# Kernel optimization log

Measured on AMD Instinct MI355X. Metric: run time of the kernel, lower is better.

Reference implementation:

```python
import jax, jax.numpy as jnp
import numpy as np

N, D, H = 8192, 64, 128
GRID = 256
RADIUS2 = 9  # radius=3 squared


def setup_inputs() -> dict:
    key = jax.random.key(0)
    ks = jax.random.split(key, 9)
    s = lambda k, shape, scale: jax.random.normal(k, shape, dtype=jnp.float32) * scale
    return {
        "positions": jax.random.randint(ks[0], (N, 2), 0, GRID, dtype=jnp.int32),
        "states": s(ks[1], (N, D), 0.1),
        "h": s(ks[2], (N, H), 0.1),
        "c": s(ks[3], (N, H), 0.1),
        "W_ih": s(ks[4], (4 * H, 2 * D), 1.0 / np.sqrt(2 * D)),
        "W_hh": s(ks[5], (4 * H, H), 1.0 / np.sqrt(H)),
        "b": s(ks[6], (4 * H,), 0.01),
        "W_out": s(ks[7], (H, D), 1.0 / np.sqrt(H)),
        "W_role": s(ks[8], (H, 3), 1.0 / np.sqrt(H)),
    }


def reference(positions, states, h, c, W_ih, W_hh, b, W_out, W_role):
    # --- neighbor gather: all-pairs distance on integer grid, radius 3 ---
    d = positions[:, None, :] - positions[None, :, :]          # [N,N,2]
    dist2 = jnp.sum(d * d, axis=-1)                            # [N,N] int32
    mask = (dist2 <= RADIUS2) & (~jnp.eye(N, dtype=bool))      # exclude self
    maskf = mask.astype(states.dtype)
    cnt = jnp.sum(maskf, axis=1, keepdims=True)                # [N,1]
    # mean of neighbor states; zeros when no neighbors (matches zeros fallback)
    nbr_mean = (maskf @ states) / jnp.maximum(cnt, 1.0)        # [N,D]

    # --- per-cell LSTM memory update ---
    x = jnp.concatenate([states, nbr_mean], axis=-1)           # [N,2D]
    gates = x @ W_ih.T + h @ W_hh.T + b                        # [N,4H]
    i_g, f_g, g_g, o_g = jnp.split(gates, 4, axis=-1)
    c_new = jax.nn.sigmoid(f_g) * c + jax.nn.sigmoid(i_g) * jnp.tanh(g_g)
    h_new = jax.nn.sigmoid(o_g) * jnp.tanh(c_new)              # [N,H]

    new_states = h_new @ W_out                                 # [N,D]
    role_probs = jax.nn.softmax(h_new @ W_role, axis=-1)       # [N,3]
    return new_states, role_probs
```

## Files before the change

kernel.cpp:

```cpp
#include <hip/hip_runtime.h>
#include <hip/hip_bf16.h>
#include <math.h>

#define N_CELLS 8192
#define D_DIM 64
#define H_DIM 128
#define GRID_SZ 256
#define NBINS (GRID_SZ * GRID_SZ)
#define BUCKET_CAP 16

typedef short bf16x8 __attribute__((ext_vector_type(8)));
typedef float f32x4 __attribute__((ext_vector_type(4)));

static __device__ __forceinline__ short f2bf(float x) {
    __hip_bfloat16 b = __float2bfloat16(x);
    return __builtin_bit_cast(short, b);
}

__global__ __launch_bounds__(256) void clear_counts(int4* __restrict__ counts4) {
    counts4[blockIdx.x * 256 + threadIdx.x] = make_int4(0, 0, 0, 0);
}

__global__ __launch_bounds__(256) void bin_fill(const int* __restrict__ positions,
                                                int* __restrict__ counts,
                                                int* __restrict__ buckets) {
    int i = blockIdx.x * 256 + threadIdx.x;
    if (i >= N_CELLS) return;
    int p0 = positions[2 * i], p1 = positions[2 * i + 1];
    int bin = p0 * GRID_SZ + p1;
    int slot = atomicAdd(&counts[bin], 1);
    if (slot < BUCKET_CAP) buckets[bin * BUCKET_CAP + slot] = i;
}

__global__ __launch_bounds__(256) void build_xh_wcvt(const int* __restrict__ positions,
                                                     const float* __restrict__ states,
                                                     const float* __restrict__ h,
                                                     const int* __restrict__ counts,
                                                     const int* __restrict__ buckets,
                                                     const float* __restrict__ Wih,
                                                     const float* __restrict__ Whh,
                                                     __hip_bfloat16* __restrict__ xh,
                                                     __hip_bfloat16* __restrict__ Wb) {
    int tid = threadIdx.x;
    if (blockIdx.x >= 2048) {
        int idx4 = (blockIdx.x - 2048) * 256 + tid;
        int gp = idx4 >> 6, k4 = (idx4 & 63) << 2;
        int group = gp >> 6, c6 = gp & 63, gate = c6 >> 4, hl = c6 & 15;
        int orig = gate * 128 + group * 16 + hl;
        float4 v = (k4 < 128) ? *(const float4*)(Wih + orig * 128 + k4)
                              : *(const float4*)(Whh + orig * 128 + (k4 - 128));
        short4 o = make_short4(f2bf(v.x), f2bf(v.y), f2bf(v.z), f2bf(v.w));
        *(short4*)((short*)Wb + gp * 256 + k4) = o;
        return;
    }
    int wave = tid >> 6;
    int lane = tid & 63;
    int i = blockIdx.x * 4 + wave;
    int p0 = positions[2 * i], p1 = positions[2 * i + 1];

    float acc = 0.0f;
    int cnt = 0;
    #pragma unroll
    for (int da = -3; da <= 3; ++da) {
        int q0 = p0 + da;
        if (q0 < 0 || q0 >= GRID_SZ) continue;
        int maxdb2 = 9 - da * da;
        #pragma unroll
        for (int db = -3; db <= 3; ++db) {
            if (db * db > maxdb2) continue;
            int q1 = p1 + db;
            if (q1 < 0 || q1 >= GRID_SZ) continue;
            int bin = q0 * GRID_SZ + q1;
            int c = counts[bin];
            if (c > BUCKET_CAP) c = BUCKET_CAP;
            for (int s = 0; s < c; ++s) {
                int j = buckets[bin * BUCKET_CAP + s];
                if (j == i) continue;
                cnt++;
                acc += states[j * D_DIM + lane];
            }
        }
    }
    float nbr = (cnt > 0) ? acc / (float)cnt : 0.0f;

    __hip_bfloat16* row = xh + (size_t)i * 256;
    row[lane]       = __float2bfloat16(states[i * D_DIM + lane]);
    row[64 + lane]  = __float2bfloat16(nbr);
    row[128 + lane] = __float2bfloat16(h[i * H_DIM + lane]);
    row[192 + lane] = __float2bfloat16(h[i * H_DIM + 64 + lane]);
}

__global__ __launch_bounds__(512) void mega(const __hip_bfloat16* __restrict__ xh,
                                            const __hip_bfloat16* __restrict__ Wb,
                                            const float* __restrict__ bias,
                                            const float* __restrict__ c_in,
                                            const float* __restrict__ W_out,
                                            const float* __restrict__ W_role,
                                            float* __restrict__ out) {
    __shared__ char smem[69632];
    char* As = smem;
    char* Bs = smem + 4096;
    char* Hl   = smem;
    char* Wohi = smem + 8192;
    char* Wolo = smem + 24576;
    char* Wr   = smem + 40960;

    const int tid  = threadIdx.x;
    const int lane = tid & 63;
    const int wid  = tid >> 6;
    const int wrow = wid >> 2, wcol = wid & 3;
    const int n0 = blockIdx.x * 32;

    const char* aG = (const char*)xh;
    const char* bG = (const char*)Wb;

    f32x4 acc[8] = {};

    for (int kc = 0; kc < 4; ++kc) {
        if (kc) __syncthreads();
        if (tid < 256) {
            int row = tid >> 3, slot = (tid & 7) << 4;
            __builtin_amdgcn_global_load_lds(
                (const __attribute__((address_space(1))) void*)(aG + (size_t)(n0 + row) * 512 + kc * 128 + (slot ^ ((row & 7) << 4))),
                (__attribute__((address_space(3))) void*)(As + row * 128 + slot), 16, 0, 0);
        }
        #pragma unroll
        for (int e = 0; e < 8; ++e) {
            int u = e * 512 + tid;
            int row = u >> 3, slot = (u & 7) << 4;
            __builtin_amdgcn_global_load_lds(
                (const __attribute__((address_space(1))) void*)(bG + (size_t)row * 512 + kc * 128 + (slot ^ ((row & 7) << 4))),
                (__attribute__((address_space(3))) void*)(Bs + row * 128 + slot), 16, 0, 0);
        }
        __syncthreads();

        #pragma unroll
        for (int ks = 0; ks < 2; ++ks) {
            int kb = ks * 64 + ((lane >> 4) << 4);
            int arow = wrow * 16 + (lane & 15);
            bf16x8 av = *(const bf16x8*)(As + arow * 128 + (kb ^ ((arow & 7) << 4)));
            #pragma unroll
            for (int ni = 0; ni < 8; ++ni) {
                int brow = wcol * 128 + ni * 16 + (lane & 15);
                bf16x8 bv = *(const bf16x8*)(Bs + brow * 128 + (kb ^ ((brow & 7) << 4)));
                acc[ni] = __builtin_amdgcn_mfma_f32_16x16x32_bf16(av, bv, acc[ni], 0, 0, 0);
            }
        }
    }
    __syncthreads();

    #pragma unroll
    for (int e = 0; e < 16; ++e) {
        int u = e * 512 + tid;
        int hh = u >> 6, d = u & 63;
        float w = W_out[u];
        float whi = __bfloat162float(__float2bfloat16(w));
        int off = d * 256 + ((hh * 2) ^ ((d & 7) << 4));
        *(short*)(Wohi + off) = f2bf(whi);
        *(short*)(Wolo + off) = f2bf(w - whi);
    }
    #pragma unroll
    for (int e = 0; e < 4; ++e) {
        int u = e * 512 + tid;
        int r = u >> 7, hh = u & 127;
        float w = (r < 3) ? W_role[hh * 3 + r] : 0.0f;
        *(short*)(Wr + r * 256 + ((hh * 2) ^ ((r & 7) << 4))) = f2bf(w);
    }

    #pragma unroll
    for (int b = 0; b < 2; ++b) {
        int hg = (2 * wcol + b) * 16 + (lane & 15);
        float bi = bias[hg], bff = bias[128 + hg], bgg = bias[256 + hg], boo = bias[384 + hg];
        #pragma unroll
        for (int r = 0; r < 4; ++r) {
            int ml = wrow * 16 + ((lane >> 4) << 2) + r;
            float ig = acc[b * 4 + 0][r] + bi;
            float fg = acc[b * 4 + 1][r] + bff;
            float gg = acc[b * 4 + 2][r] + bgg;
            float og = acc[b * 4 + 3][r] + boo;
            float cv = c_in[(size_t)(n0 + ml) * H_DIM + hg];
            float si = 1.0f / (1.0f + expf(-ig));
            float sf = 1.0f / (1.0f + expf(-fg));
            float so = 1.0f / (1.0f + expf(-og));
            float hn = so * tanhf(sf * cv + si * tanhf(gg));
            *(short*)(Hl + ml * 256 + ((hg * 2) ^ ((ml & 7) << 4))) = f2bf(hn);
        }
    }
    __syncthreads();

    const int rb = wid >> 2, db = wid & 3;
    f32x4 oacc = {};
    f32x4 racc = {};
    #pragma unroll
    for (int ks = 0; ks < 4; ++ks) {
        int kb = ks * 64 + ((lane >> 4) << 4);
        int hrow = rb * 16 + (lane & 15);
        bf16x8 hv = *(const bf16x8*)(Hl + hrow * 256 + (kb ^ ((hrow & 7) << 4)));
        int drow = db * 16 + (lane & 15);
        int woff = drow * 256 + (kb ^ ((drow & 7) << 4));
        bf16x8 whi = *(const bf16x8*)(Wohi + woff);
        bf16x8 wlo = *(const bf16x8*)(Wolo + woff);
        oacc = __builtin_amdgcn_mfma_f32_16x16x32_bf16(hv, whi, oacc, 0, 0, 0);
        oacc = __builtin_amdgcn_mfma_f32_16x16x32_bf16(hv, wlo, oacc, 0, 0, 0);
        if (db == 3) {
            int rrow = lane & 15;
            bf16x8 wr = *(const bf16x8*)(Wr + rrow * 256 + (kb ^ ((rrow & 7) << 4)));
            racc = __builtin_amdgcn_mfma_f32_16x16x32_bf16(wr, hv, racc, 0, 0, 0);
        }
    }
    #pragma unroll
    for (int r = 0; r < 4; ++r) {
        int m = n0 + rb * 16 + ((lane >> 4) << 2) + r;
        out[(size_t)m * D_DIM + db * 16 + (lane & 15)] = oacc[r];
    }
    if (db == 3 && lane < 16) {
        int m = n0 + rb * 16 + lane;
        float l0 = racc[0], l1 = racc[1], l2 = racc[2];
        float mx = fmaxf(l0, fmaxf(l1, l2));
        float e0 = expf(l0 - mx), e1 = expf(l1 - mx), e2 = expf(l2 - mx);
        float s = e0 + e1 + e2;
        float* ro = out + (size_t)N_CELLS * D_DIM + (size_t)m * 3;
        ro[0] = e0 / s; ro[1] = e1 / s; ro[2] = e2 / s;
    }
}

extern "C" void kernel_launch(void* const* d_in, const int* in_sizes, int n_in,
                              void* d_out, int out_size, void* d_ws, size_t ws_size,
                              hipStream_t stream) {
    const int*   positions = (const int*)d_in[0];
    const float* states    = (const float*)d_in[1];
    const float* h         = (const float*)d_in[2];
    const float* c         = (const float*)d_in[3];
    const float* Wih       = (const float*)d_in[4];
    const float* Whh       = (const float*)d_in[5];
    const float* bias      = (const float*)d_in[6];
    const float* Wout      = (const float*)d_in[7];
    const float* Wrole     = (const float*)d_in[8];
    float* out             = (float*)d_out;

    char* ws = (char*)d_ws;
    int*            counts  = (int*)ws;
    int*            buckets = (int*)(ws + 262144);
    __hip_bfloat16* xh      = (__hip_bfloat16*)(ws + 4456448);
    __hip_bfloat16* Wb      = (__hip_bfloat16*)(ws + 8650752);

    clear_counts<<<NBINS / 1024, 256, 0, stream>>>((int4*)counts);
    bin_fill<<<N_CELLS / 256, 256, 0, stream>>>(positions, counts, buckets);
    build_xh_wcvt<<<2048 + 128, 256, 0, stream>>>(positions, states, h, counts, buckets,
                                                  Wih, Whh, xh, Wb);
    mega<<<N_CELLS / 32, 512, 0, stream>>>(xh, Wb, bias, c, Wout, Wrole, out);
}
```

Measured before the change: 40.92 us.

## Fuse neighbor gather into GEMM kernel and merge weight conversion with count clearing

The neighbor-mean gather and xh row construction move into the mega kernel, which now writes bf16 A-tiles for all 32 rows and the full K=256 directly into LDS instead of staging them through a global xh buffer. Weight conversion is combined with count clearing in a single prep kernel, cutting the launches from four to three and removing the global write and re-read of xh. The cost is larger LDS use per block (80KB), which may limit occupancy, and the gather latency now sits at the start of the GEMM kernel with fewer waves available to hide it.

```diff
diff --git a/kernel.cpp b/kernel.cpp
--- a/kernel.cpp
+++ b/kernel.cpp
@@ -17,8 +17,23 @@
     return __builtin_bit_cast(short, b);
 }
 
-__global__ __launch_bounds__(256) void clear_counts(int4* __restrict__ counts4) {
-    counts4[blockIdx.x * 256 + threadIdx.x] = make_int4(0, 0, 0, 0);
+__global__ __launch_bounds__(256) void prep(const float* __restrict__ Wih,
+                                            const float* __restrict__ Whh,
+                                            __hip_bfloat16* __restrict__ Wb,
+                                            int4* __restrict__ counts4) {
+    int tid = threadIdx.x;
+    if (blockIdx.x >= 128) {
+        counts4[(blockIdx.x - 128) * 256 + tid] = make_int4(0, 0, 0, 0);
+        return;
+    }
+    int idx4 = blockIdx.x * 256 + tid;
+    int gp = idx4 >> 6, k4 = (idx4 & 63) << 2;
+    int group = gp >> 6, c6 = gp & 63, gate = c6 >> 4, hl = c6 & 15;
+    int orig = gate * 128 + group * 16 + hl;
+    float4 v = (k4 < 128) ? *(const float4*)(Wih + orig * 128 + k4)
+                          : *(const float4*)(Whh + orig * 128 + (k4 - 128));
+    short4 o = make_short4(f2bf(v.x), f2bf(v.y), f2bf(v.z), f2bf(v.w));
+    *(short4*)((short*)Wb + gp * 256 + k4) = o;
 }
 
 __global__ __launch_bounds__(256) void bin_fill(const int* __restrict__ positions,
@@ -32,74 +47,20 @@
     if (slot < BUCKET_CAP) buckets[bin * BUCKET_CAP + slot] = i;
 }
 
-__global__ __launch_bounds__(256) void build_xh_wcvt(const int* __restrict__ positions,
-                                                     const float* __restrict__ states,
-                                                     const float* __restrict__ h,
-                                                     const int* __restrict__ counts,
-                                                     const int* __restrict__ buckets,
-                                                     const float* __restrict__ Wih,
-                                                     const float* __restrict__ Whh,
-                                                     __hip_bfloat16* __restrict__ xh,
-                                                     __hip_bfloat16* __restrict__ Wb) {
-    int tid = threadIdx.x;
-    if (blockIdx.x >= 2048) {
-        int idx4 = (blockIdx.x - 2048) * 256 + tid;
-        int gp = idx4 >> 6, k4 = (idx4 & 63) << 2;
-        int group = gp >> 6, c6 = gp & 63, gate = c6 >> 4, hl = c6 & 15;
-        int orig = gate * 128 + group * 16 + hl;
-        float4 v = (k4 < 128) ? *(const float4*)(Wih + orig * 128 + k4)
-                              : *(const float4*)(Whh + orig * 128 + (k4 - 128));
-        short4 o = make_short4(f2bf(v.x), f2bf(v.y), f2bf(v.z), f2bf(v.w));
-        *(short4*)((short*)Wb + gp * 256 + k4) = o;
-        return;
-    }
-    int wave = tid >> 6;
-    int lane = tid & 63;
-    int i = blockIdx.x * 4 + wave;
-    int p0 = positions[2 * i], p1 = positions[2 * i + 1];
-
-    float acc = 0.0f;
-    int cnt = 0;
-    #pragma unroll
-    for (int da = -3; da <= 3; ++da) {
-        int q0 = p0 + da;
-        if (q0 < 0 || q0 >= GRID_SZ) continue;
-        int maxdb2 = 9 - da * da;
-        #pragma unroll
-        for (int db = -3; db <= 3; ++db) {
-            if (db * db > maxdb2) continue;
-            int q1 = p1 + db;
-            if (q1 < 0 || q1 >= GRID_SZ) continue;
-            int bin = q0 * GRID_SZ + q1;
-            int c = counts[bin];
-            if (c > BUCKET_CAP) c = BUCKET_CAP;
-            for (int s = 0; s < c; ++s) {
-                int j = buckets[bin * BUCKET_CAP + s];
-                if (j == i) continue;
-                cnt++;
-                acc += states[j * D_DIM + lane];
-            }
-        }
-    }
-    float nbr = (cnt > 0) ? acc / (float)cnt : 0.0f;
-
-    __hip_bfloat16* row = xh + (size_t)i * 256;
-    row[lane]       = __float2bfloat16(states[i * D_DIM + lane]);
-    row[64 + lane]  = __float2bfloat16(nbr);
-    row[128 + lane] = __float2bfloat16(h[i * H_DIM + lane]);
-    row[192 + lane] = __float2bfloat16(h[i * H_DIM + 64 + lane]);
-}
-
-__global__ __launch_bounds__(512) void mega(const __hip_bfloat16* __restrict__ xh,
+__global__ __launch_bounds__(512) void mega(const int* __restrict__ positions,
+                                            const float* __restrict__ states,
+                                            const float* __restrict__ h,
+                                            const int* __restrict__ counts,
+                                            const int* __restrict__ buckets,
                                             const __hip_bfloat16* __restrict__ Wb,
                                             const float* __restrict__ bias,
                                             const float* __restrict__ c_in,
                                             const float* __restrict__ W_out,
                                             const float* __restrict__ W_role,
                                             float* __restrict__ out) {
-    __shared__ char smem[69632];
+    __shared__ char smem[81920];
     char* As = smem;
-    char* Bs = smem + 4096;
+    char* Bs = smem + 16384;
     char* Hl   = smem;
     char* Wohi = smem + 8192;
     char* Wolo = smem + 24576;
@@ -111,19 +72,54 @@
     const int wrow = wid >> 2, wcol = wid & 3;
     const int n0 = blockIdx.x * 32;
 
-    const char* aG = (const char*)xh;
+    const int DA[29] = {-3,-2,-2,-2,-2,-2,-1,-1,-1,-1,-1, 0, 0, 0, 0, 0, 0, 0, 1, 1, 1, 1, 1, 2, 2, 2, 2, 2, 3};
+    const int DB[29] = { 0,-2,-1, 0, 1, 2,-2,-1, 0, 1, 2,-3,-2,-1, 0, 1, 2, 3,-2,-1, 0, 1, 2,-2,-1, 0, 1, 2, 0};
+
+    #pragma unroll
+    for (int cc = 0; cc < 4; ++cc) {
+        int i = n0 + wid * 4 + cc;
+        int p0 = positions[2 * i], p1 = positions[2 * i + 1];
+        int bc[29], bbase[29];
+        #pragma unroll
+        for (int t = 0; t < 29; ++t) {
+            int q0 = p0 + DA[t], q1 = p1 + DB[t];
+            bool ok = ((unsigned)q0 < GRID_SZ) && ((unsigned)q1 < GRID_SZ);
+            int bin = q0 * GRID_SZ + q1;
+            bc[t] = ok ? counts[bin] : 0;
+            bbase[t] = bin * BUCKET_CAP;
+        }
+        float acc = 0.0f;
+        int cnt = 0;
+        #pragma unroll
+        for (int t = 0; t < 29; ++t) {
+            int c = bc[t] < BUCKET_CAP ? bc[t] : BUCKET_CAP;
+            for (int s = 0; s < c; ++s) {
+                int j = buckets[bbase[t] + s];
+                if (j == i) continue;
+                cnt++;
+                acc += states[j * D_DIM + lane];
+            }
+        }
+        float nbr = (cnt > 0) ? acc / (float)cnt : 0.0f;
+        float sv = states[i * D_DIM + lane];
+        float h0 = h[i * H_DIM + lane];
+        float h1 = h[i * H_DIM + 64 + lane];
+
+        int ml = wid * 4 + cc;
+        int ro = ml * 512;
+        int swz = (ml & 7) << 4;
+        *(short*)(As + ro + ((2 * lane) ^ swz))       = f2bf(sv);
+        *(short*)(As + ro + ((128 + 2 * lane) ^ swz)) = f2bf(nbr);
+        *(short*)(As + ro + ((256 + 2 * lane) ^ swz)) = f2bf(h0);
+        *(short*)(As + ro + ((384 + 2 * lane) ^ swz)) = f2bf(h1);
+    }
+
     const char* bG = (const char*)Wb;
 
     f32x4 acc[8] = {};
 
     for (int kc = 0; kc < 4; ++kc) {
         if (kc) __syncthreads();
-        if (tid < 256) {
-            int row = tid >> 3, slot = (tid & 7) << 4;
-            __builtin_amdgcn_global_load_lds(
-                (const __attribute__((address_space(1))) void*)(aG + (size_t)(n0 + row) * 512 + kc * 128 + (slot ^ ((row & 7) << 4))),
-                (__attribute__((address_space(3))) void*)(As + row * 128 + slot), 16, 0, 0);
-        }
         #pragma unroll
         for (int e = 0; e < 8; ++e) {
             int u = e * 512 + tid;
@@ -136,9 +132,10 @@
 
         #pragma unroll
         for (int ks = 0; ks < 2; ++ks) {
+            int arow = wrow * 16 + (lane & 15);
+            int kbb = kc * 128 + ks * 64 + ((lane >> 4) << 4);
+            bf16x8 av = *(const bf16x8*)(As + arow * 512 + (kbb ^ ((arow & 7) << 4)));
             int kb = ks * 64 + ((lane >> 4) << 4);
-            int arow = wrow * 16 + (lane & 15);
-            bf16x8 av = *(const bf16x8*)(As + arow * 128 + (kb ^ ((arow & 7) << 4)));
             #pragma unroll
             for (int ni = 0; ni < 8; ++ni) {
                 int brow = wcol * 128 + ni * 16 + (lane & 15);
@@ -241,12 +238,10 @@
     char* ws = (char*)d_ws;
     int*            counts  = (int*)ws;
     int*            buckets = (int*)(ws + 262144);
-    __hip_bfloat16* xh      = (__hip_bfloat16*)(ws + 4456448);
-    __hip_bfloat16* Wb      = (__hip_bfloat16*)(ws + 8650752);
-
-    clear_counts<<<NBINS / 1024, 256, 0, stream>>>((int4*)counts);
+    __hip_bfloat16* Wb      = (__hip_bfloat16*)(ws + 4456448);
+
+    prep<<<192, 256, 0, stream>>>(Wih, Whh, Wb, (int4*)counts);
     bin_fill<<<N_CELLS / 256, 256, 0, stream>>>(positions, counts, buckets);
-    build_xh_wcvt<<<2048 + 128, 256, 0, stream>>>(positions, states, h, counts, buckets,
-                                                  Wih, Whh, xh, Wb);
-    mega<<<N_CELLS / 32, 512, 0, stream>>>(xh, Wb, bias, c, Wout, Wrole, out);
-}
+    mega<<<N_CELLS / 32, 512, 0, stream>>>(positions, states, h, counts, buckets,
+                                           Wb, bias, c, Wout, Wrole, out);
+}
```

Measured after the change: 42.06 us. 1.03x slower.

## Split fused LSTM kernel into gate and output kernels, precompute output weights

Applied to the files above, without the earlier changes.

The single mega kernel is split into mega1, which computes the gate GEMM and LSTM cell and writes h_new in bf16 to workspace, and mega2, which computes the output and role projections. Each mega1 block now covers half the gates, so there are twice as many blocks, and the A tile is read straight into registers instead of LDS. The W_out hi/lo and W_role bf16 conversion moves out of every block into a shared prep kernel, which also clears the counts. This trades an extra launch and an h_new global round trip for more parallelism and no repeated per-block weight conversion.

```diff
diff --git a/kernel.cpp b/kernel.cpp
--- a/kernel.cpp
+++ b/kernel.cpp
@@ -17,8 +17,43 @@
     return __builtin_bit_cast(short, b);
 }
 
-__global__ __launch_bounds__(256) void clear_counts(int4* __restrict__ counts4) {
-    counts4[blockIdx.x * 256 + threadIdx.x] = make_int4(0, 0, 0, 0);
+__global__ __launch_bounds__(256) void prep(const float* __restrict__ Wih,
+                                            const float* __restrict__ Whh,
+                                            const float* __restrict__ W_out,
+                                            const float* __restrict__ W_role,
+                                            __hip_bfloat16* __restrict__ Wb,
+                                            __hip_bfloat16* __restrict__ Wohi,
+                                            __hip_bfloat16* __restrict__ Wolo,
+                                            __hip_bfloat16* __restrict__ Wr,
+                                            int4* __restrict__ counts4) {
+    int tid = threadIdx.x, b = blockIdx.x;
+    if (b < 128) {
+        int idx4 = b * 256 + tid;
+        int gp = idx4 >> 6, k4 = (idx4 & 63) << 2;
+        int group = gp >> 6, c6 = gp & 63, gate = c6 >> 4, hl = c6 & 15;
+        int orig = gate * 128 + group * 16 + hl;
+        float4 v = (k4 < 128) ? *(const float4*)(Wih + orig * 128 + k4)
+                              : *(const float4*)(Whh + orig * 128 + (k4 - 128));
+        short4 o = make_short4(f2bf(v.x), f2bf(v.y), f2bf(v.z), f2bf(v.w));
+        *(short4*)((short*)Wb + gp * 256 + k4) = o;
+    } else if (b < 192) {
+        counts4[(b - 128) * 256 + tid] = make_int4(0, 0, 0, 0);
+    } else if (b < 224) {
+        int u = (b - 192) * 256 + tid;
+        int hh = u >> 6, d = u & 63;
+        float w = W_out[u];
+        float whi = __bfloat162float(__float2bfloat16(w));
+        Wohi[d * 128 + hh] = __float2bfloat16(whi);
+        Wolo[d * 128 + hh] = __float2bfloat16(w - whi);
+    } else {
+        #pragma unroll
+        for (int e = 0; e < 8; ++e) {
+            int u = e * 256 + tid;
+            int r = u >> 7, hh = u & 127;
+            float w = (r < 3) ? W_role[hh * 3 + r] : 0.0f;
+            Wr[r * 128 + hh] = __float2bfloat16(w);
+        }
+    }
 }
 
 __global__ __launch_bounds__(256) void bin_fill(const int* __restrict__ positions,
@@ -32,29 +67,14 @@
     if (slot < BUCKET_CAP) buckets[bin * BUCKET_CAP + slot] = i;
 }
 
-__global__ __launch_bounds__(256) void build_xh_wcvt(const int* __restrict__ positions,
-                                                     const float* __restrict__ states,
-                                                     const float* __restrict__ h,
-                                                     const int* __restrict__ counts,
-                                                     const int* __restrict__ buckets,
-                                                     const float* __restrict__ Wih,
-                                                     const float* __restrict__ Whh,
-                                                     __hip_bfloat16* __restrict__ xh,
-                                                     __hip_bfloat16* __restrict__ Wb) {
-    int tid = threadIdx.x;
-    if (blockIdx.x >= 2048) {
-        int idx4 = (blockIdx.x - 2048) * 256 + tid;
-        int gp = idx4 >> 6, k4 = (idx4 & 63) << 2;
-        int group = gp >> 6, c6 = gp & 63, gate = c6 >> 4, hl = c6 & 15;
-        int orig = gate * 128 + group * 16 + hl;
-        float4 v = (k4 < 128) ? *(const float4*)(Wih + orig * 128 + k4)
-                              : *(const float4*)(Whh + orig * 128 + (k4 - 128));
-        short4 o = make_short4(f2bf(v.x), f2bf(v.y), f2bf(v.z), f2bf(v.w));
-        *(short4*)((short*)Wb + gp * 256 + k4) = o;
-        return;
-    }
-    int wave = tid >> 6;
-    int lane = tid & 63;
+__global__ __launch_bounds__(256) void build_xh(const int* __restrict__ positions,
+                                                const float* __restrict__ states,
+                                                const float* __restrict__ h,
+                                                const int* __restrict__ counts,
+                                                const int* __restrict__ buckets,
+                                                __hip_bfloat16* __restrict__ xh) {
+    int wave = threadIdx.x >> 6;
+    int lane = threadIdx.x & 63;
     int i = blockIdx.x * 4 + wave;
     int p0 = positions[2 * i], p1 = positions[2 * i + 1];
 
@@ -90,46 +110,47 @@
     row[192 + lane] = __float2bfloat16(h[i * H_DIM + 64 + lane]);
 }
 
-__global__ __launch_bounds__(512) void mega(const __hip_bfloat16* __restrict__ xh,
-                                            const __hip_bfloat16* __restrict__ Wb,
-                                            const float* __restrict__ bias,
-                                            const float* __restrict__ c_in,
-                                            const float* __restrict__ W_out,
-                                            const float* __restrict__ W_role,
-                                            float* __restrict__ out) {
-    __shared__ char smem[69632];
-    char* As = smem;
-    char* Bs = smem + 4096;
-    char* Hl   = smem;
-    char* Wohi = smem + 8192;
-    char* Wolo = smem + 24576;
-    char* Wr   = smem + 40960;
+__global__ __launch_bounds__(256) void mega1(const __hip_bfloat16* __restrict__ xh,
+                                             const __hip_bfloat16* __restrict__ Wb,
+                                             const float* __restrict__ bias,
+                                             const float* __restrict__ c_in,
+                                             __hip_bfloat16* __restrict__ h_new) {
+    __shared__ char Bs[32768];
 
     const int tid  = threadIdx.x;
     const int lane = tid & 63;
     const int wid  = tid >> 6;
-    const int wrow = wid >> 2, wcol = wid & 3;
-    const int n0 = blockIdx.x * 32;
-
-    const char* aG = (const char*)xh;
+    const int wrow = wid >> 1, wcol = wid & 1;
+    const int nb = blockIdx.x >> 1, gb = blockIdx.x & 1;
+    const int n0 = nb * 32, g0 = gb * 256;
+
+    const short* xr = (const short*)xh + (size_t)(n0 + wrow * 16 + (lane & 15)) * 256 + ((lane >> 4) << 3);
+    bf16x8 av[8];
+    #pragma unroll
+    for (int z = 0; z < 8; ++z) av[z] = *(const bf16x8*)(xr + z * 32);
+
+    float cv[2][4];
+    #pragma unroll
+    for (int b = 0; b < 2; ++b) {
+        int hg = (gb * 4 + 2 * wcol + b) * 16 + (lane & 15);
+        #pragma unroll
+        for (int r = 0; r < 4; ++r) {
+            int ml = wrow * 16 + ((lane >> 4) << 2) + r;
+            cv[b][r] = c_in[(size_t)(n0 + ml) * H_DIM + hg];
+        }
+    }
+
     const char* bG = (const char*)Wb;
-
     f32x4 acc[8] = {};
 
     for (int kc = 0; kc < 4; ++kc) {
         if (kc) __syncthreads();
-        if (tid < 256) {
-            int row = tid >> 3, slot = (tid & 7) << 4;
-            __builtin_amdgcn_global_load_lds(
-                (const __attribute__((address_space(1))) void*)(aG + (size_t)(n0 + row) * 512 + kc * 128 + (slot ^ ((row & 7) << 4))),
-                (__attribute__((address_space(3))) void*)(As + row * 128 + slot), 16, 0, 0);
-        }
         #pragma unroll
         for (int e = 0; e < 8; ++e) {
-            int u = e * 512 + tid;
+            int u = e * 256 + tid;
             int row = u >> 3, slot = (u & 7) << 4;
             __builtin_amdgcn_global_load_lds(
-                (const __attribute__((address_space(1))) void*)(bG + (size_t)row * 512 + kc * 128 + (slot ^ ((row & 7) << 4))),
+                (const __attribute__((address_space(1))) void*)(bG + (size_t)(g0 + row) * 512 + kc * 128 + (slot ^ ((row & 7) << 4))),
                 (__attribute__((address_space(3))) void*)(Bs + row * 128 + slot), 16, 0, 0);
         }
         __syncthreads();
@@ -137,39 +158,18 @@
         #pragma unroll
         for (int ks = 0; ks < 2; ++ks) {
             int kb = ks * 64 + ((lane >> 4) << 4);
-            int arow = wrow * 16 + (lane & 15);
-            bf16x8 av = *(const bf16x8*)(As + arow * 128 + (kb ^ ((arow & 7) << 4)));
             #pragma unroll
             for (int ni = 0; ni < 8; ++ni) {
                 int brow = wcol * 128 + ni * 16 + (lane & 15);
                 bf16x8 bv = *(const bf16x8*)(Bs + brow * 128 + (kb ^ ((brow & 7) << 4)));
-                acc[ni] = __builtin_amdgcn_mfma_f32_16x16x32_bf16(av, bv, acc[ni], 0, 0, 0);
+                acc[ni] = __builtin_amdgcn_mfma_f32_16x16x32_bf16(av[kc * 2 + ks], bv, acc[ni], 0, 0, 0);
             }
         }
     }
-    __syncthreads();
-
-    #pragma unroll
-    for (int e = 0; e < 16; ++e) {
-        int u = e * 512 + tid;
-        int hh = u >> 6, d = u & 63;
-        float w = W_out[u];
-        float whi = __bfloat162float(__float2bfloat16(w));
-        int off = d * 256 + ((hh * 2) ^ ((d & 7) << 4));
-        *(short*)(Wohi + off) = f2bf(whi);
-        *(short*)(Wolo + off) = f2bf(w - whi);
-    }
-    #pragma unroll
-    for (int e = 0; e < 4; ++e) {
-        int u = e * 512 + tid;
-        int r = u >> 7, hh = u & 127;
-        float w = (r < 3) ? W_role[hh * 3 + r] : 0.0f;
-        *(short*)(Wr + r * 256 + ((hh * 2) ^ ((r & 7) << 4))) = f2bf(w);
-    }
 
     #pragma unroll
     for (int b = 0; b < 2; ++b) {
-        int hg = (2 * wcol + b) * 16 + (lane & 15);
+        int hg = (gb * 4 + 2 * wcol + b) * 16 + (lane & 15);
         float bi = bias[hg], bff = bias[128 + hg], bgg = bias[256 + hg], boo = bias[384 + hg];
         #pragma unroll
         for (int r = 0; r < 4; ++r) {
@@ -178,43 +178,85 @@
             float fg = acc[b * 4 + 1][r] + bff;
             float gg = acc[b * 4 + 2][r] + bgg;
             float og = acc[b * 4 + 3][r] + boo;
-            float cv = c_in[(size_t)(n0 + ml) * H_DIM + hg];
             float si = 1.0f / (1.0f + expf(-ig));
             float sf = 1.0f / (1.0f + expf(-fg));
             float so = 1.0f / (1.0f + expf(-og));
-            float hn = so * tanhf(sf * cv + si * tanhf(gg));
-            *(short*)(Hl + ml * 256 + ((hg * 2) ^ ((ml & 7) << 4))) = f2bf(hn);
-        }
-    }
+            float hn = so * tanhf(sf * cv[b][r] + si * tanhf(gg));
+            h_new[(size_t)(n0 + ml) * H_DIM + hg] = __float2bfloat16(hn);
+        }
+    }
+}
+
+__global__ __launch_bounds__(256) void mega2(const __hip_bfloat16* __restrict__ h_new,
+                                             const __hip_bfloat16* __restrict__ Wohi,
+                                             const __hip_bfloat16* __restrict__ Wolo,
+                                             const __hip_bfloat16* __restrict__ Wr,
+                                             float* __restrict__ out) {
+    __shared__ char smem[36864];
+
+    const int tid  = threadIdx.x;
+    const int lane = tid & 63;
+    const int w    = tid >> 6;
+    const int n0   = blockIdx.x * 16;
+
+    const char* hiG = (const char*)Wohi;
+    const char* loG = (const char*)Wolo;
+    const char* wrG = (const char*)Wr;
+
+    #pragma unroll
+    for (int e = 0; e < 4; ++e) {
+        int u = e * 256 + tid;
+        int row = u >> 4, slot = (u & 15) << 4;
+        __builtin_amdgcn_global_load_lds(
+            (const __attribute__((address_space(1))) void*)(hiG + row * 256 + (slot ^ ((row & 7) << 4))),
+            (__attribute__((address_space(3))) void*)(smem + row * 256 + slot), 16, 0, 0);
+    }
+    #pragma unroll
+    for (int e = 0; e < 4; ++e) {
+        int u = e * 256 + tid;
+        int row = u >> 4, slot = (u & 15) << 4;
+        __builtin_amdgcn_global_load_lds(
+            (const __attribute__((address_space(1))) void*)(loG + row * 256 + (slot ^ ((row & 7) << 4))),
+            (__attribute__((address_space(3))) void*)(smem + 16384 + row * 256 + slot), 16, 0, 0);
+    }
+    {
+        int row = tid >> 4, slot = (tid & 15) << 4;
+        __builtin_amdgcn_global_load_lds(
+            (const __attribute__((address_space(1))) void*)(wrG + row * 256 + (slot ^ ((row & 7) << 4))),
+            (__attribute__((address_space(3))) void*)(smem + 32768 + row * 256 + slot), 16, 0, 0);
+    }
+
+    const short* hr = (const short*)h_new + (size_t)(n0 + (lane & 15)) * H_DIM + ((lane >> 4) << 3);
+    bf16x8 hv[4];
+    #pragma unroll
+    for (int ks = 0; ks < 4; ++ks) hv[ks] = *(const bf16x8*)(hr + ks * 32);
+
     __syncthreads();
 
-    const int rb = wid >> 2, db = wid & 3;
     f32x4 oacc = {};
     f32x4 racc = {};
     #pragma unroll
     for (int ks = 0; ks < 4; ++ks) {
         int kb = ks * 64 + ((lane >> 4) << 4);
-        int hrow = rb * 16 + (lane & 15);
-        bf16x8 hv = *(const bf16x8*)(Hl + hrow * 256 + (kb ^ ((hrow & 7) << 4)));
-        int drow = db * 16 + (lane & 15);
+        int drow = w * 16 + (lane & 15);
         int woff = drow * 256 + (kb ^ ((drow & 7) << 4));
-        bf16x8 whi = *(const bf16x8*)(Wohi + woff);
-        bf16x8 wlo = *(const bf16x8*)(Wolo + woff);
-        oacc = __builtin_amdgcn_mfma_f32_16x16x32_bf16(hv, whi, oacc, 0, 0, 0);
-        oacc = __builtin_amdgcn_mfma_f32_16x16x32_bf16(hv, wlo, oacc, 0, 0, 0);
-        if (db == 3) {
+        bf16x8 whi = *(const bf16x8*)(smem + woff);
+        bf16x8 wlo = *(const bf16x8*)(smem + 16384 + woff);
+        oacc = __builtin_amdgcn_mfma_f32_16x16x32_bf16(hv[ks], whi, oacc, 0, 0, 0);
+        oacc = __builtin_amdgcn_mfma_f32_16x16x32_bf16(hv[ks], wlo, oacc, 0, 0, 0);
+        if (w == 0) {
             int rrow = lane & 15;
-            bf16x8 wr = *(const bf16x8*)(Wr + rrow * 256 + (kb ^ ((rrow & 7) << 4)));
-            racc = __builtin_amdgcn_mfma_f32_16x16x32_bf16(wr, hv, racc, 0, 0, 0);
+            bf16x8 wr = *(const bf16x8*)(smem + 32768 + rrow * 256 + (kb ^ ((rrow & 7) << 4)));
+            racc = __builtin_amdgcn_mfma_f32_16x16x32_bf16(wr, hv[ks], racc, 0, 0, 0);
         }
     }
     #pragma unroll
     for (int r = 0; r < 4; ++r) {
-        int m = n0 + rb * 16 + ((lane >> 4) << 2) + r;
-        out[(size_t)m * D_DIM + db * 16 + (lane & 15)] = oacc[r];
-    }
-    if (db == 3 && lane < 16) {
-        int m = n0 + rb * 16 + lane;
+        int m = n0 + ((lane >> 4) << 2) + r;
+        out[(size_t)m * D_DIM + w * 16 + (lane & 15)] = oacc[r];
+    }
+    if (w == 0 && lane < 16) {
+        int m = n0 + lane;
         float l0 = racc[0], l1 = racc[1], l2 = racc[2];
         float mx = fmaxf(l0, fmaxf(l1, l2));
         float e0 = expf(l0 - mx), e1 = expf(l1 - mx), e2 = expf(l2 - mx);
@@ -243,10 +285,14 @@
     int*            buckets = (int*)(ws + 262144);
     __hip_bfloat16* xh      = (__hip_bfloat16*)(ws + 4456448);
     __hip_bfloat16* Wb      = (__hip_bfloat16*)(ws + 8650752);
-
-    clear_counts<<<NBINS / 1024, 256, 0, stream>>>((int4*)counts);
+    __hip_bfloat16* Wohi    = (__hip_bfloat16*)(ws + 8912896);
+    __hip_bfloat16* Wolo    = (__hip_bfloat16*)(ws + 8929280);
+    __hip_bfloat16* Wr      = (__hip_bfloat16*)(ws + 8945664);
+    __hip_bfloat16* h_new   = (__hip_bfloat16*)(ws + 8949760);
+
+    prep<<<225, 256, 0, stream>>>(Wih, Whh, Wout, Wrole, Wb, Wohi, Wolo, Wr, (int4*)counts);
     bin_fill<<<N_CELLS / 256, 256, 0, stream>>>(positions, counts, buckets);
-    build_xh_wcvt<<<2048 + 128, 256, 0, stream>>>(positions, states, h, counts, buckets,
-                                                  Wih, Whh, xh, Wb);
-    mega<<<N_CELLS / 32, 512, 0, stream>>>(xh, Wb, bias, c, Wout, Wrole, out);
-}
+    build_xh<<<N_CELLS / 4, 256, 0, stream>>>(positions, states, h, counts, buckets, xh);
+    mega1<<<512, 256, 0, stream>>>(xh, Wb, bias, c, h_new);
+    mega2<<<512, 256, 0, stream>>>(h_new, Wohi, Wolo, Wr, out);
+}
```

Result: slower. 43.89 us (+7.3%).

## Parallelize neighbor-bin probing across lanes and move weight conversion into prep kernel

Applied to the files above, without the earlier changes.

Each of the 29 bins inside the radius-3 disk is now probed by its own lane, which loads the bin count and the first four bucket entries in parallel. A ballot then walks only the non-empty bins, broadcasting indices with shuffles. This replaces the serial per-bin count and bucket loads that every lane used to repeat. The bf16 weight conversion moves out of build_xh into the count-clearing kernel, so it runs alongside the clear. The cost is some added shuffle and ballot overhead.

```diff
diff --git a/kernel.cpp b/kernel.cpp
--- a/kernel.cpp
+++ b/kernel.cpp
@@ -17,8 +17,23 @@
     return __builtin_bit_cast(short, b);
 }
 
-__global__ __launch_bounds__(256) void clear_counts(int4* __restrict__ counts4) {
-    counts4[blockIdx.x * 256 + threadIdx.x] = make_int4(0, 0, 0, 0);
+__global__ __launch_bounds__(256) void prep(const float* __restrict__ Wih,
+                                            const float* __restrict__ Whh,
+                                            __hip_bfloat16* __restrict__ Wb,
+                                            int4* __restrict__ counts4) {
+    int tid = threadIdx.x, b = blockIdx.x;
+    if (b >= 128) {
+        counts4[(b - 128) * 256 + tid] = make_int4(0, 0, 0, 0);
+        return;
+    }
+    int idx4 = b * 256 + tid;
+    int gp = idx4 >> 6, k4 = (idx4 & 63) << 2;
+    int group = gp >> 6, c6 = gp & 63, gate = c6 >> 4, hl = c6 & 15;
+    int orig = gate * 128 + group * 16 + hl;
+    float4 v = (k4 < 128) ? *(const float4*)(Wih + orig * 128 + k4)
+                          : *(const float4*)(Whh + orig * 128 + (k4 - 128));
+    short4 o = make_short4(f2bf(v.x), f2bf(v.y), f2bf(v.z), f2bf(v.w));
+    *(short4*)((short*)Wb + gp * 256 + k4) = o;
 }
 
 __global__ __launch_bounds__(256) void bin_fill(const int* __restrict__ positions,
@@ -32,52 +47,57 @@
     if (slot < BUCKET_CAP) buckets[bin * BUCKET_CAP + slot] = i;
 }
 
-__global__ __launch_bounds__(256) void build_xh_wcvt(const int* __restrict__ positions,
-                                                     const float* __restrict__ states,
-                                                     const float* __restrict__ h,
-                                                     const int* __restrict__ counts,
-                                                     const int* __restrict__ buckets,
-                                                     const float* __restrict__ Wih,
-                                                     const float* __restrict__ Whh,
-                                                     __hip_bfloat16* __restrict__ xh,
-                                                     __hip_bfloat16* __restrict__ Wb) {
-    int tid = threadIdx.x;
-    if (blockIdx.x >= 2048) {
-        int idx4 = (blockIdx.x - 2048) * 256 + tid;
-        int gp = idx4 >> 6, k4 = (idx4 & 63) << 2;
-        int group = gp >> 6, c6 = gp & 63, gate = c6 >> 4, hl = c6 & 15;
-        int orig = gate * 128 + group * 16 + hl;
-        float4 v = (k4 < 128) ? *(const float4*)(Wih + orig * 128 + k4)
-                              : *(const float4*)(Whh + orig * 128 + (k4 - 128));
-        short4 o = make_short4(f2bf(v.x), f2bf(v.y), f2bf(v.z), f2bf(v.w));
-        *(short4*)((short*)Wb + gp * 256 + k4) = o;
-        return;
-    }
-    int wave = tid >> 6;
-    int lane = tid & 63;
+__global__ __launch_bounds__(256) void build_xh(const int* __restrict__ positions,
+                                                const float* __restrict__ states,
+                                                const float* __restrict__ h,
+                                                const int* __restrict__ counts,
+                                                const int* __restrict__ buckets,
+                                                __hip_bfloat16* __restrict__ xh) {
+    int wave = threadIdx.x >> 6;
+    int lane = threadIdx.x & 63;
     int i = blockIdx.x * 4 + wave;
     int p0 = positions[2 * i], p1 = positions[2 * i + 1];
 
+    int t = lane;
+    int da, db;
+    if (t == 0)      { da = -3; db = 0; }
+    else if (t < 6)  { da = -2; db = t - 3; }
+    else if (t < 11) { da = -1; db = t - 8; }
+    else if (t < 18) { da = 0;  db = t - 14; }
+    else if (t < 23) { da = 1;  db = t - 20; }
+    else if (t < 28) { da = 2;  db = t - 25; }
+    else             { da = 3;  db = 0; }
+
+    int q0 = p0 + da, q1 = p1 + db;
+    bool ok = (lane < 29) && ((unsigned)q0 < GRID_SZ) && ((unsigned)q1 < GRID_SZ);
+    int bin = q0 * GRID_SZ + q1;
+
+    int cl = 0;
+    int4 jv = make_int4(0, 0, 0, 0);
+    if (ok) {
+        cl = counts[bin];
+        jv = *(const int4*)(buckets + bin * BUCKET_CAP);
+        if (cl > BUCKET_CAP) cl = BUCKET_CAP;
+    }
+
+    unsigned long long act = __ballot(cl > 0);
     float acc = 0.0f;
     int cnt = 0;
-    #pragma unroll
-    for (int da = -3; da <= 3; ++da) {
-        int q0 = p0 + da;
-        if (q0 < 0 || q0 >= GRID_SZ) continue;
-        int maxdb2 = 9 - da * da;
-        #pragma unroll
-        for (int db = -3; db <= 3; ++db) {
-            if (db * db > maxdb2) continue;
-            int q1 = p1 + db;
-            if (q1 < 0 || q1 >= GRID_SZ) continue;
-            int bin = q0 * GRID_SZ + q1;
-            int c = counts[bin];
-            if (c > BUCKET_CAP) c = BUCKET_CAP;
-            for (int s = 0; s < c; ++s) {
-                int j = buckets[bin * BUCKET_CAP + s];
-                if (j == i) continue;
-                cnt++;
-                acc += states[j * D_DIM + lane];
+    while (act) {
+        int tb = __ffsll(act) - 1;
+        act &= act - 1;
+        int ct = __shfl(cl, tb);
+        int j0 = __shfl(jv.x, tb), j1 = __shfl(jv.y, tb);
+        int j2 = __shfl(jv.z, tb), j3 = __shfl(jv.w, tb);
+        if (j0 != i)           { cnt++; acc += states[j0 * D_DIM + lane]; }
+        if (ct > 1 && j1 != i) { cnt++; acc += states[j1 * D_DIM + lane]; }
+        if (ct > 2 && j2 != i) { cnt++; acc += states[j2 * D_DIM + lane]; }
+        if (ct > 3 && j3 != i) { cnt++; acc += states[j3 * D_DIM + lane]; }
+        if (ct > 4) {
+            int bb = __shfl(bin, tb) * BUCKET_CAP;
+            for (int s = 4; s < ct; ++s) {
+                int j = buckets[bb + s];
+                if (j != i) { cnt++; acc += states[j * D_DIM + lane]; }
             }
         }
     }
@@ -244,9 +264,8 @@
     __hip_bfloat16* xh      = (__hip_bfloat16*)(ws + 4456448);
     __hip_bfloat16* Wb      = (__hip_bfloat16*)(ws + 8650752);
 
-    clear_counts<<<NBINS / 1024, 256, 0, stream>>>((int4*)counts);
+    prep<<<192, 256, 0, stream>>>(Wih, Whh, Wb, (int4*)counts);
     bin_fill<<<N_CELLS / 256, 256, 0, stream>>>(positions, counts, buckets);
-    build_xh_wcvt<<<2048 + 128, 256, 0, stream>>>(positions, states, h, counts, buckets,
-                                                  Wih, Whh, xh, Wb);
+    build_xh<<<N_CELLS / 4, 256, 0, stream>>>(positions, states, h, counts, buckets, xh);
     mega<<<N_CELLS / 32, 512, 0, stream>>>(xh, Wb, bias, c, Wout, Wrole, out);
 }
```

Measured after the change: 34.59 us. 15.5% less time.
